# Optimization experiments

Hardware: AMD Instinct MI355X
Metric: run time of the kernel (lower is better)

Reference implementation:

```python
import jax, jax.numpy as jnp
import numpy as np

K_LEN, I_LEN, DIM = 1024, 8192, 128


def setup_inputs() -> dict:
    key = jax.random.key(0)
    k1, k2 = jax.random.split(key)
    kernel = jax.random.normal(k1, (K_LEN, DIM), dtype=jnp.float32)
    x = jax.random.normal(k2, (I_LEN, DIM), dtype=jnp.float32)
    return {"kernel": kernel, "x": x}


def _cost_matrix(kernel, x):
    # squared Euclidean pairwise distances, (K, I), via GEMM form
    k2 = jnp.sum(kernel * kernel, axis=-1)  # (K,)
    x2 = jnp.sum(x * x, axis=-1)            # (I,)
    c = k2[:, None] + x2[None, :] - 2.0 * (kernel @ x.T)
    return jnp.maximum(c, 0.0)


def _acc_matrix(c):
    # DTW DP: D[i,j] = c[i,j] + min(D[i-1,j-1], D[i-1,j], D[i,j-1])
    # Row recurrence solved per-row with a (min,+) prefix scan:
    #   e[j] = min(D_prev[j-1], D_prev[j]) + c[j]   (e[0] = D_prev[0] + c[0])
    #   D[j] = S[j] + cummin(e - S),  S = cumsum(c_row)
    row0 = jnp.cumsum(c[0])

    def step(prev, c_row):
        m = jnp.concatenate([prev[:1], jnp.minimum(prev[:-1], prev[1:])])
        e = m + c_row
        S = jnp.cumsum(c_row)
        row = S + jax.lax.cummin(e - S)
        return row, row

    _, rows = jax.lax.scan(step, row0, c[1:])
    return jnp.concatenate([row0[None, :], rows], axis=0)  # (K, I)


def _backtrack(D):
    # tslearn-style backtracking from (K-1, I-1) to (0, 0).
    # Candidate order [diag, up, left]; argmin ties pick first (diag),
    # matching numpy.argmin used by tslearn. Out-of-range -> +inf border.
    K, I = D.shape
    Dp = jnp.full((K + 1, I + 1), jnp.inf, dtype=D.dtype).at[1:, 1:].set(D)
    L = K + I - 1  # max possible path length

    def step(carry, _):
        k, i, fin = carry
        emit = (k, i, jnp.logical_not(fin))
        fin2 = fin | ((k == 0) & (i == 0))
        cand = jnp.stack([Dp[k, i], Dp[k, i + 1], Dp[k + 1, i]])
        a = jnp.argmin(cand)
        nk = jnp.where(fin2, k, k - (a != 2).astype(k.dtype))
        ni = jnp.where(fin2, i, i - (a != 1).astype(i.dtype))
        return (nk, ni, fin2), emit

    init = (jnp.int32(K - 1), jnp.int32(I - 1), jnp.bool_(False))
    _, (ks, iss, valid) = jax.lax.scan(step, init, None, length=L)
    return ks, iss, valid


def reference(kernel, x):
    # Path search uses detached tensors in the original module.
    c = jax.lax.stop_gradient(_cost_matrix(kernel, x))
    D = _acc_matrix(c)
    ks, iss, valid = _backtrack(D)
    # sum of squared diffs along the optimal alignment path (gather + reduce)
    d2 = jnp.sum((kernel[ks] - x[iss]) ** 2, axis=-1)  # (L,)
    return jnp.sum(jnp.where(valid, d2, 0.0))
```

## Files before the change

kernel.cpp:

```cpp
#include <hip/hip_runtime.h>
#include <hip/hip_bf16.h>

typedef unsigned short ushort_t;
typedef unsigned int uint_t;

#define KL 1024
#define IL 8192
#define DIMV 128
#define NS 16
#define NB 258
#define NIT 269
#define SSH (8256*64)
#define GATE 416
#define INF __builtin_inff()

typedef __attribute__((ext_vector_type(8))) short v8s;
typedef __attribute__((ext_vector_type(4))) float v4f;

__global__ __launch_bounds__(256) void knorms(
    const float* __restrict__ kern, const float* __restrict__ xx,
    float* __restrict__ x2, float* __restrict__ k2, int* __restrict__ flags) {
  if (blockIdx.x == 0 && threadIdx.x < NS) flags[threadIdx.x] = 0;
  const int lane = threadIdx.x & 63;
  const int row = blockIdx.x * 4 + (threadIdx.x >> 6);
  const float* src;
  float* dst;
  if (row < IL) { src = xx + (size_t)row * DIMV; dst = x2 + row; }
  else          { src = kern + (size_t)(row - IL) * DIMV; dst = k2 + (row - IL); }
  float2 v = *(const float2*)(src + lane * 2);
  float ss = v.x * v.x + v.y * v.y;
  #pragma unroll
  for (int off = 32; off > 0; off >>= 1) ss += __shfl_down(ss, off, 64);
  if (lane == 0) *dst = ss;
}

__device__ __forceinline__ v8s pack_bf16x8(float4 a, float4 b) {
  union { unsigned int u[4]; v8s v; } r;
  union { __hip_bfloat162 h; unsigned int u; } t;
  t.h = __float22bfloat162_rn(make_float2(a.x, a.y)); r.u[0] = t.u;
  t.h = __float22bfloat162_rn(make_float2(a.z, a.w)); r.u[1] = t.u;
  t.h = __float22bfloat162_rn(make_float2(b.x, b.y)); r.u[2] = t.u;
  t.h = __float22bfloat162_rn(make_float2(b.z, b.w)); r.u[3] = t.u;
  return r.v;
}

__global__ __launch_bounds__(256) void kgemm(
    const float* __restrict__ kern, const float* __restrict__ xx,
    const float* __restrict__ x2, const float* __restrict__ k2,
    ushort_t* __restrict__ c_h) {
  __shared__ float ctile[64 * 64];
  const int T = threadIdx.x;
  const int w = T >> 6;
  const int lane = T & 63;
  const int lo = lane & 15;
  const int hi = lane >> 4;
  const int i0 = blockIdx.x * 64;
  const int s  = blockIdx.y;
  const int kr0 = s * 64;

  v4f acc[4] = {};
  #pragma unroll
  for (int ks = 0; ks < 4; ks++) {
    const int k = ks * 32 + hi * 8;
    const float* bp = xx + (size_t)(i0 + w * 16 + lo) * DIMV + k;
    v8s bf = pack_bf16x8(*(const float4*)bp, *(const float4*)(bp + 4));
    #pragma unroll
    for (int rt = 0; rt < 4; rt++) {
      const float* ap = kern + (size_t)(kr0 + rt * 16 + lo) * DIMV + k;
      v8s af = pack_bf16x8(*(const float4*)ap, *(const float4*)(ap + 4));
      acc[rt] = __builtin_amdgcn_mfma_f32_16x16x32_bf16(af, bf, acc[rt], 0, 0, 0);
    }
  }
  const float x2v = x2[i0 + w * 16 + lo];
  const int n_local = w * 16 + lo;
  #pragma unroll
  for (int rt = 0; rt < 4; rt++) {
    float4 k2f = *(const float4*)&k2[kr0 + rt * 16 + hi * 4];
    #pragma unroll
    for (int q = 0; q < 4; q++) {
      const int m_local = rt * 16 + hi * 4 + q;
      float cval = fmaxf((&k2f.x)[q] + x2v - 2.f * acc[rt][q], 0.f);
      ctile[n_local * 64 + ((m_local + 2 * n_local) & 63)] = cval;
    }
  }
  __syncthreads();
  _Float16* ob = (_Float16*)(c_h + (size_t)s * SSH);
  #pragma unroll
  for (int q = 0; q < 32; q++) {
    int tt = w + q * 4;
    int di = tt - lane;
    if (tt <= 126 && di >= 0 && di < 64) {
      int t = i0 + tt;
      ob[((size_t)(t >> 1) * 64 + lane) * 2 + (t & 1)] =
          (_Float16)ctile[di * 64 + ((lane + 2 * di) & 63)];
    }
  }
}

__device__ __forceinline__ float dpp_wave_shr1(float oldv, float src) {
  return __int_as_float(__builtin_amdgcn_update_dpp(
      __float_as_int(oldv), __float_as_int(src), 0x138, 0xF, 0xF, false));
}
__device__ __forceinline__ float dpp_wave_rol1(float src) {
  return __int_as_float(__builtin_amdgcn_update_dpp(
      __float_as_int(src), __float_as_int(src), 0x134, 0xF, 0xF, false));
}
__device__ __forceinline__ float dpp_wave_shl1(float oldv, float src) {
  return __int_as_float(__builtin_amdgcn_update_dpp(
      __float_as_int(oldv), __float_as_int(src), 0x130, 0xF, 0xF, false));
}

__global__ __launch_bounds__(384) void kdp(
    const ushort_t* __restrict__ c_h, float* __restrict__ bound,
    int* __restrict__ flags, float* __restrict__ out) {
  __shared__ uint_t cbuf[4 * 2 * 1024];
  __shared__ float ring[4 * 4 * 32];
  __shared__ float feed[4 * 32];
  const int g = blockIdx.x;
  const int wv = threadIdx.x >> 6;
  const int lane = threadIdx.x & 63;
  const int sb = g * 4;

  float Dcur = INF, Dul = INF, Bout = INF;
  int fchk = 0, fpend = 0;
  float rfeed = INF;
  const float* bin = bound + (size_t)(sb > 0 ? sb - 1 : 0) * IL;
  float* bout3 = bound + (size_t)(sb + 3) * IL;

  if (wv == 4) {
    const char* gs = (const char*)(c_h + (size_t)sb * SSH);
    uint_t* dst = cbuf;
    #pragma unroll
    for (int q = 0; q < 4; q++)
      __builtin_amdgcn_global_load_lds(
          (const __attribute__((address_space(1))) void*)(gs + (size_t)q * 1024 + lane * 16),
          (__attribute__((address_space(3))) void*)(dst + q * 256 + lane * 4), 16, 0, 0);
  } else if (wv == 5) {
    if (g > 0) {
      int f;
      do { f = __hip_atomic_load(&flags[sb - 1], __ATOMIC_RELAXED, __HIP_MEMORY_SCOPE_AGENT); } while (f < GATE);
      fchk = f; fpend = f;
      if (lane < 32) {
        feed[lane]      = __hip_atomic_load(&bin[lane],      __ATOMIC_RELAXED, __HIP_MEMORY_SCOPE_AGENT);
        feed[32 + lane] = __hip_atomic_load(&bin[32 + lane], __ATOMIC_RELAXED, __HIP_MEMORY_SCOPE_AGENT);
        rfeed           = __hip_atomic_load(&bin[64 + lane], __ATOMIC_RELAXED, __HIP_MEMORY_SCOPE_AGENT);
      }
    } else {
      if (lane < 32) { feed[lane] = INF; feed[32+lane] = INF; feed[64+lane] = INF; feed[96+lane] = INF; }
    }
  } else if (wv < 4) {
    if (g == 0 && wv == 0 && lane == 0) Dcur = 0.f;
  }
  __syncthreads();

  for (int i = 0; i < NIT; i++) {
    if (wv < 4) {
      const int W = i - 3 * wv;
      if (W >= 0 && W < NB) {
        const uint_t* lc = cbuf + (wv * 2 + (W & 1)) * 1024 + lane;
        uint_t lv[16];
        #pragma unroll
        for (int tp = 0; tp < 16; tp++) lv[tp] = lc[tp * 64];
        float Bv = (wv == 0) ? feed[(W & 3) * 32 + (lane & 31)]
                             : ring[(wv - 1) * 128 + (W & 3) * 32 + (lane & 31)];
        float cvv[32];
        #pragma unroll
        for (int tp = 0; tp < 16; tp++) {
          union { uint_t u; _Float16 h[2]; } cu; cu.u = lv[tp];
          cvv[2 * tp]     = (float)cu.h[0];
          cvv[2 * tp + 1] = (float)cu.h[1];
        }
        if (W >= 2 && W < 256) {
          #pragma unroll
          for (int tt = 0; tt < 32; tt++) {
            float Dup = dpp_wave_shr1(Bv, Dcur);
            float m1 = fminf(Dul, Dcur);
            Bv = dpp_wave_rol1(Bv);
            Dcur = cvv[tt] + fminf(m1, Dup);
            Dul = Dup;
            Bout = dpp_wave_shl1(Dcur, Bout);
          }
        } else {
          const int t0 = W * 32;
          #pragma unroll
          for (int tt = 0; tt < 32; tt++) {
            const int t = t0 + tt;
            float Dup = dpp_wave_shr1(Bv, Dcur);
            float m1 = fminf(Dul, Dcur);
            Bv = dpp_wave_rol1(Bv);
            float Dnew = cvv[tt] + fminf(m1, Dup);
            const bool alo = (t >= lane);
            const bool ahi = (t - lane < IL);
            if (alo) Dul = Dup;
            if (alo && ahi) Dcur = Dnew;
            Bout = dpp_wave_shl1(Dcur, Bout);
          }
        }
        if (lane >= 32) {
          const int slot = (lane == 63) ? (W - 1) : (W - 2);
          if (slot >= 0)
            ring[wv * 128 + ((slot & 3) << 5) + ((lane + 1) & 31)] = Bout;
        }
      }
    } else if (wv == 4) {
      #pragma unroll
      for (int k = 0; k < 4; k++) {
        const int B = i + 1 - 3 * k;
        if (B >= 0 && B < NB) {
          const char* gs = (const char*)(c_h + (size_t)(sb + k) * SSH) + (size_t)B * 4096;
          uint_t* dst = cbuf + (k * 2 + (B & 1)) * 1024;
          #pragma unroll
          for (int q = 0; q < 4; q++)
            __builtin_amdgcn_global_load_lds(
                (const __attribute__((address_space(1))) void*)(gs + (size_t)q * 1024 + lane * 16),
                (__attribute__((address_space(3))) void*)(dst + q * 256 + lane * 4), 16, 0, 0);
        }
      }
    } else {
      if (g > 0) {
        if (fpend > fchk) fchk = fpend;
        const int Fw = i + 2;
        if (Fw >= 2 && Fw <= 255 && lane < 32) feed[(Fw & 3) * 32 + lane] = rfeed;
        const int Fl = i + 3;
        if (Fl <= 255) {
          const int need = 32 * (Fl + 1);
          if (fchk < need) {
            int f;
            do { f = __hip_atomic_load(&flags[sb - 1], __ATOMIC_RELAXED, __HIP_MEMORY_SCOPE_AGENT); } while (f < need);
            fchk = f;
          }
          if (lane < 32)
            rfeed = __hip_atomic_load(&bin[32 * Fl + lane], __ATOMIC_RELAXED, __HIP_MEMORY_SCOPE_AGENT);
        }
        fpend = __hip_atomic_load(&flags[sb - 1], __ATOMIC_RELAXED, __HIP_MEMORY_SCOPE_AGENT);
      }
      if (g < 3) {
        const int E = i - 12;
        if (E >= 0 && E < 256 && lane < 32) {
          float bv2 = ring[3 * 128 + (E & 3) * 32 + lane];
          __hip_atomic_store(&bout3[32 * E + lane], bv2, __ATOMIC_RELAXED, __HIP_MEMORY_SCOPE_AGENT);
        }
        const int Ep = i - 13;
        if (Ep >= 0 && Ep < 256 && lane == 0)
          __hip_atomic_store(&flags[sb + 3], 32 * Ep + 32, __ATOMIC_RELAXED, __HIP_MEMORY_SCOPE_AGENT);
      }
    }
    __syncthreads();
  }
  if (g == 3 && wv == 3 && lane == 63) out[0] = Dcur;
}

extern "C" void kernel_launch(void* const* d_in, const int* in_sizes, int n_in,
                              void* d_out, int out_size, void* d_ws, size_t ws_size,
                              hipStream_t stream) {
  const float* kern = (const float*)d_in[0];
  const float* xx   = (const float*)d_in[1];
  char* ws = (char*)d_ws;
  const size_t OFF_X2 = (size_t)NS * SSH * 2;
  const size_t OFF_K2 = OFF_X2 + (size_t)IL * 4;
  const size_t OFF_BD = OFF_K2 + (size_t)KL * 4;
  const size_t OFF_FL = OFF_BD + (size_t)NS * IL * 4;
  ushort_t* c_h  = (ushort_t*)ws;
  float* x2    = (float*)(ws + OFF_X2);
  float* k2    = (float*)(ws + OFF_K2);
  float* bnd   = (float*)(ws + OFF_BD);
  int*   flags = (int*)(ws + OFF_FL);

  knorms<<<(IL + KL) / 4, 256, 0, stream>>>(kern, xx, x2, k2, flags);
  kgemm<<<dim3(IL / 64, NS), 256, 0, stream>>>(kern, xx, x2, k2, c_h);
  kdp<<<4, 384, 0, stream>>>(c_h, bnd, flags, (float*)d_out);
}
```

Measured before the change: 405.3 us.

## Replace per-iteration block barriers with LDS flag-based producer/consumer sync in DP kernel

The DP wavefront kernel no longer advances every wave in lockstep with __syncthreads each iteration. Each compute, loader, feed and export wave now runs its own loop and waits on per-stage counters in LDS. The cost buffer goes from double to triple buffering, and a seventh wave splits off boundary export from boundary feeding. This removes barrier stalls where one slow wave holds up all others. In exchange it adds spin-polling on LDS and needs careful memory ordering, which risks races or hangs if any flag dependency is wrong.

```diff
diff --git a/kernel.cpp b/kernel.cpp
--- a/kernel.cpp
+++ b/kernel.cpp
@@ -9,10 +9,16 @@
 #define DIMV 128
 #define NS 16
 #define NB 258
-#define NIT 269
+#define NR 267
 #define SSH (8256*64)
 #define GATE 416
+#define BIGF 0x3fffffff
 #define INF __builtin_inff()
+
+#define CF 0
+#define PF 4
+#define GF 8
+#define EF 9
 
 typedef __attribute__((ext_vector_type(8))) short v8s;
 typedef __attribute__((ext_vector_type(4))) float v4f;
@@ -110,144 +116,166 @@
       __float_as_int(oldv), __float_as_int(src), 0x130, 0xF, 0xF, false));
 }
 
-__global__ __launch_bounds__(384) void kdp(
+__device__ __forceinline__ int lds_poll_ge(int* p, int need, int cached) {
+  if (cached >= need) return cached;
+  int f;
+  do { f = __hip_atomic_load(p, __ATOMIC_RELAXED, __HIP_MEMORY_SCOPE_WORKGROUP); } while (f < need);
+  return f;
+}
+
+__global__ __launch_bounds__(448) void kdp(
     const ushort_t* __restrict__ c_h, float* __restrict__ bound,
     int* __restrict__ flags, float* __restrict__ out) {
-  __shared__ uint_t cbuf[4 * 2 * 1024];
+  __shared__ uint_t cbuf[13 * 1024];
   __shared__ float ring[4 * 4 * 32];
-  __shared__ float feed[4 * 32];
+  __shared__ float feedb[4 * 32];
+  __shared__ int flg[16];
   const int g = blockIdx.x;
   const int wv = threadIdx.x >> 6;
   const int lane = threadIdx.x & 63;
   const int sb = g * 4;
 
-  float Dcur = INF, Dul = INF, Bout = INF;
-  int fchk = 0, fpend = 0;
-  float rfeed = INF;
-  const float* bin = bound + (size_t)(sb > 0 ? sb - 1 : 0) * IL;
-  float* bout3 = bound + (size_t)(sb + 3) * IL;
-
-  if (wv == 4) {
-    const char* gs = (const char*)(c_h + (size_t)sb * SSH);
-    uint_t* dst = cbuf;
+  if (threadIdx.x < 16) {
+    int v = -1;
+    if (threadIdx.x == GF && g == 0) v = BIGF;
+    if (threadIdx.x == EF && g == 3) v = BIGF;
+    flg[threadIdx.x] = v;
+  }
+  if (wv == 1) { feedb[lane] = INF; feedb[64 + lane] = INF; }
+  __syncthreads();
+
+  if (wv < 4) {
+    const int k = wv;
+    float Dcur = (g == 0 && k == 0 && lane == 0) ? 0.f : INF;
+    float Dul = INF, Bout = INF;
+    int fc = -1, fp = -1;
+    int fe = (g == 3 && k == 3) ? BIGF : -1;
+    int s3 = 0;
+    for (int W = 0; W < NB; W++) {
+      fc = lds_poll_ge(&flg[CF + k], W, fc);
+      if (k == 0) {
+        if (W < 256) fp = lds_poll_ge(&flg[GF], W, fp);
+      } else {
+        int pn = W + 2; if (pn > 257) pn = 257;
+        fp = lds_poll_ge(&flg[PF + k - 1], pn, fp);
+      }
+      fe = lds_poll_ge(&flg[(k < 3) ? (PF + k + 1) : EF], W - 4, fe);
+      const uint_t* lc = cbuf + (k * 3 + s3) * 1024 + lane;
+      uint_t lv[16];
+      #pragma unroll
+      for (int tp = 0; tp < 16; tp++) lv[tp] = lc[tp * 64];
+      float Bv = (k == 0) ? feedb[(W & 3) * 32 + (lane & 31)]
+                          : ring[(k - 1) * 128 + (W & 3) * 32 + (lane & 31)];
+      float cvv[32];
+      #pragma unroll
+      for (int tp = 0; tp < 16; tp++) {
+        union { uint_t u; _Float16 h[2]; } cu; cu.u = lv[tp];
+        cvv[2 * tp]     = (float)cu.h[0];
+        cvv[2 * tp + 1] = (float)cu.h[1];
+      }
+      if (W >= 2 && W < 256) {
+        #pragma unroll
+        for (int tt = 0; tt < 32; tt++) {
+          float Dup = dpp_wave_shr1(Bv, Dcur);
+          float m1 = fminf(Dul, Dcur);
+          Bv = dpp_wave_rol1(Bv);
+          Dcur = cvv[tt] + fminf(m1, Dup);
+          Dul = Dup;
+          Bout = dpp_wave_shl1(Dcur, Bout);
+        }
+      } else {
+        const int t0 = W * 32;
+        #pragma unroll
+        for (int tt = 0; tt < 32; tt++) {
+          const int t = t0 + tt;
+          float Dup = dpp_wave_shr1(Bv, Dcur);
+          float m1 = fminf(Dul, Dcur);
+          Bv = dpp_wave_rol1(Bv);
+          float Dnew = cvv[tt] + fminf(m1, Dup);
+          const bool alo = (t >= lane);
+          const bool ahi = (t - lane < IL);
+          if (alo) Dul = Dup;
+          if (alo && ahi) Dcur = Dnew;
+          Bout = dpp_wave_shl1(Dcur, Bout);
+        }
+      }
+      if (lane >= 32) {
+        const int slot = (lane == 63) ? (W - 1) : (W - 2);
+        if (slot >= 0) ring[k * 128 + ((slot & 3) << 5) + ((lane + 1) & 31)] = Bout;
+      }
+      __hip_atomic_store(&flg[PF + k], W, __ATOMIC_RELEASE, __HIP_MEMORY_SCOPE_WORKGROUP);
+      s3 = (s3 == 2) ? 0 : s3 + 1;
+    }
+    if (g == 3 && k == 3 && lane == 63) out[0] = Dcur;
+  } else if (wv == 4) {
+    int fpk[4] = {-1, -1, -1, -1};
+    for (int R = 0; R < NR; R++) {
+      const int sl = R % 3;
+      #pragma unroll
+      for (int k = 0; k < 4; k++) {
+        const int B = R - 3 * k;
+        const bool v = (B >= 0) && (B < NB);
+        if (v) fpk[k] = lds_poll_ge(&flg[PF + k], B - 3, fpk[k]);
+        const int slot = v ? (k * 3 + sl) : 12;
+        const char* src = (const char*)(c_h + (size_t)(sb + k) * SSH) + (size_t)(v ? B : 0) * 4096;
+        uint_t* dst = cbuf + slot * 1024;
+        #pragma unroll
+        for (int q = 0; q < 4; q++)
+          __builtin_amdgcn_global_load_lds(
+              (const __attribute__((address_space(1))) void*)(src + (size_t)q * 1024 + lane * 16),
+              (__attribute__((address_space(3))) void*)(dst + q * 256 + lane * 4), 16, 0, 0);
+      }
+      asm volatile("s_waitcnt vmcnt(16)" ::: "memory");
+      #pragma unroll
+      for (int k = 0; k < 4; k++) {
+        int c = (R - 1) - 3 * k; if (c > 257) c = 257;
+        if (c >= 0)
+          __hip_atomic_store(&flg[CF + k], c, __ATOMIC_RELAXED, __HIP_MEMORY_SCOPE_WORKGROUP);
+      }
+    }
+    asm volatile("s_waitcnt vmcnt(0)" ::: "memory");
     #pragma unroll
-    for (int q = 0; q < 4; q++)
-      __builtin_amdgcn_global_load_lds(
-          (const __attribute__((address_space(1))) void*)(gs + (size_t)q * 1024 + lane * 16),
-          (__attribute__((address_space(3))) void*)(dst + q * 256 + lane * 4), 16, 0, 0);
+    for (int k = 0; k < 4; k++)
+      __hip_atomic_store(&flg[CF + k], 257, __ATOMIC_RELAXED, __HIP_MEMORY_SCOPE_WORKGROUP);
   } else if (wv == 5) {
     if (g > 0) {
-      int f;
-      do { f = __hip_atomic_load(&flags[sb - 1], __ATOMIC_RELAXED, __HIP_MEMORY_SCOPE_AGENT); } while (f < GATE);
-      fchk = f; fpend = f;
-      if (lane < 32) {
-        feed[lane]      = __hip_atomic_load(&bin[lane],      __ATOMIC_RELAXED, __HIP_MEMORY_SCOPE_AGENT);
-        feed[32 + lane] = __hip_atomic_load(&bin[32 + lane], __ATOMIC_RELAXED, __HIP_MEMORY_SCOPE_AGENT);
-        rfeed           = __hip_atomic_load(&bin[64 + lane], __ATOMIC_RELAXED, __HIP_MEMORY_SCOPE_AGENT);
-      }
-    } else {
-      if (lane < 32) { feed[lane] = INF; feed[32+lane] = INF; feed[64+lane] = INF; feed[96+lane] = INF; }
-    }
-  } else if (wv < 4) {
-    if (g == 0 && wv == 0 && lane == 0) Dcur = 0.f;
-  }
-  __syncthreads();
-
-  for (int i = 0; i < NIT; i++) {
-    if (wv < 4) {
-      const int W = i - 3 * wv;
-      if (W >= 0 && W < NB) {
-        const uint_t* lc = cbuf + (wv * 2 + (W & 1)) * 1024 + lane;
-        uint_t lv[16];
-        #pragma unroll
-        for (int tp = 0; tp < 16; tp++) lv[tp] = lc[tp * 64];
-        float Bv = (wv == 0) ? feed[(W & 3) * 32 + (lane & 31)]
-                             : ring[(wv - 1) * 128 + (W & 3) * 32 + (lane & 31)];
-        float cvv[32];
-        #pragma unroll
-        for (int tp = 0; tp < 16; tp++) {
-          union { uint_t u; _Float16 h[2]; } cu; cu.u = lv[tp];
-          cvv[2 * tp]     = (float)cu.h[0];
-          cvv[2 * tp + 1] = (float)cu.h[1];
+      const float* bin = bound + (size_t)(sb - 1) * IL;
+      int fg;
+      do { fg = __hip_atomic_load(&flags[sb - 1], __ATOMIC_RELAXED, __HIP_MEMORY_SCOPE_AGENT); } while (fg < GATE);
+      int fp0 = -1;
+      for (int F = 0; F <= 254; F += 2) {
+        const int need = 32 * F + 64;
+        while (fg < need)
+          fg = __hip_atomic_load(&flags[sb - 1], __ATOMIC_RELAXED, __HIP_MEMORY_SCOPE_AGENT);
+        float r = __hip_atomic_load(&bin[32 * F + lane], __ATOMIC_RELAXED, __HIP_MEMORY_SCOPE_AGENT);
+        fp0 = lds_poll_ge(&flg[PF + 0], F - 3, fp0);
+        feedb[(F & 3) * 32 + lane] = r;
+        __hip_atomic_store(&flg[GF], F + 1, __ATOMIC_RELEASE, __HIP_MEMORY_SCOPE_WORKGROUP);
+      }
+    }
+  } else {
+    if (g < 3) {
+      float* bout3 = bound + (size_t)(sb + 3) * IL;
+      int fp3 = -1;
+      for (int E = 0; E < 256; E++) {
+        int pn = E + 2; if (pn > 257) pn = 257;
+        fp3 = lds_poll_ge(&flg[PF + 3], pn, fp3);
+        float bv = ring[3 * 128 + (E & 3) * 32 + (lane & 31)];
+        asm volatile("s_waitcnt lgkmcnt(0)" ::: "memory");
+        __hip_atomic_store(&flg[EF], E, __ATOMIC_RELAXED, __HIP_MEMORY_SCOPE_WORKGROUP);
+        if (lane < 32)
+          __hip_atomic_store(&bout3[32 * E + lane], bv, __ATOMIC_RELAXED, __HIP_MEMORY_SCOPE_AGENT);
+        if (E >= 2) {
+          asm volatile("s_waitcnt vmcnt(3)" ::: "memory");
+          if (lane == 0)
+            __hip_atomic_store(&flags[sb + 3], 32 * (E - 2) + 32, __ATOMIC_RELAXED, __HIP_MEMORY_SCOPE_AGENT);
         }
-        if (W >= 2 && W < 256) {
-          #pragma unroll
-          for (int tt = 0; tt < 32; tt++) {
-            float Dup = dpp_wave_shr1(Bv, Dcur);
-            float m1 = fminf(Dul, Dcur);
-            Bv = dpp_wave_rol1(Bv);
-            Dcur = cvv[tt] + fminf(m1, Dup);
-            Dul = Dup;
-            Bout = dpp_wave_shl1(Dcur, Bout);
-          }
-        } else {
-          const int t0 = W * 32;
-          #pragma unroll
-          for (int tt = 0; tt < 32; tt++) {
-            const int t = t0 + tt;
-            float Dup = dpp_wave_shr1(Bv, Dcur);
-            float m1 = fminf(Dul, Dcur);
-            Bv = dpp_wave_rol1(Bv);
-            float Dnew = cvv[tt] + fminf(m1, Dup);
-            const bool alo = (t >= lane);
-            const bool ahi = (t - lane < IL);
-            if (alo) Dul = Dup;
-            if (alo && ahi) Dcur = Dnew;
-            Bout = dpp_wave_shl1(Dcur, Bout);
-          }
-        }
-        if (lane >= 32) {
-          const int slot = (lane == 63) ? (W - 1) : (W - 2);
-          if (slot >= 0)
-            ring[wv * 128 + ((slot & 3) << 5) + ((lane + 1) & 31)] = Bout;
-        }
-      }
-    } else if (wv == 4) {
-      #pragma unroll
-      for (int k = 0; k < 4; k++) {
-        const int B = i + 1 - 3 * k;
-        if (B >= 0 && B < NB) {
-          const char* gs = (const char*)(c_h + (size_t)(sb + k) * SSH) + (size_t)B * 4096;
-          uint_t* dst = cbuf + (k * 2 + (B & 1)) * 1024;
-          #pragma unroll
-          for (int q = 0; q < 4; q++)
-            __builtin_amdgcn_global_load_lds(
-                (const __attribute__((address_space(1))) void*)(gs + (size_t)q * 1024 + lane * 16),
-                (__attribute__((address_space(3))) void*)(dst + q * 256 + lane * 4), 16, 0, 0);
-        }
-      }
-    } else {
-      if (g > 0) {
-        if (fpend > fchk) fchk = fpend;
-        const int Fw = i + 2;
-        if (Fw >= 2 && Fw <= 255 && lane < 32) feed[(Fw & 3) * 32 + lane] = rfeed;
-        const int Fl = i + 3;
-        if (Fl <= 255) {
-          const int need = 32 * (Fl + 1);
-          if (fchk < need) {
-            int f;
-            do { f = __hip_atomic_load(&flags[sb - 1], __ATOMIC_RELAXED, __HIP_MEMORY_SCOPE_AGENT); } while (f < need);
-            fchk = f;
-          }
-          if (lane < 32)
-            rfeed = __hip_atomic_load(&bin[32 * Fl + lane], __ATOMIC_RELAXED, __HIP_MEMORY_SCOPE_AGENT);
-        }
-        fpend = __hip_atomic_load(&flags[sb - 1], __ATOMIC_RELAXED, __HIP_MEMORY_SCOPE_AGENT);
-      }
-      if (g < 3) {
-        const int E = i - 12;
-        if (E >= 0 && E < 256 && lane < 32) {
-          float bv2 = ring[3 * 128 + (E & 3) * 32 + lane];
-          __hip_atomic_store(&bout3[32 * E + lane], bv2, __ATOMIC_RELAXED, __HIP_MEMORY_SCOPE_AGENT);
-        }
-        const int Ep = i - 13;
-        if (Ep >= 0 && Ep < 256 && lane == 0)
-          __hip_atomic_store(&flags[sb + 3], 32 * Ep + 32, __ATOMIC_RELAXED, __HIP_MEMORY_SCOPE_AGENT);
-      }
-    }
-    __syncthreads();
-  }
-  if (g == 3 && wv == 3 && lane == 63) out[0] = Dcur;
+      }
+      asm volatile("s_waitcnt vmcnt(0)" ::: "memory");
+      if (lane == 0)
+        __hip_atomic_store(&flags[sb + 3], IL, __ATOMIC_RELAXED, __HIP_MEMORY_SCOPE_AGENT);
+    }
+  }
 }
 
 extern "C" void kernel_launch(void* const* d_in, const int* in_sizes, int n_in,
@@ -268,5 +296,5 @@
 
   knorms<<<(IL + KL) / 4, 256, 0, stream>>>(kern, xx, x2, k2, flags);
   kgemm<<<dim3(IL / 64, NS), 256, 0, stream>>>(kern, xx, x2, k2, c_h);
-  kdp<<<4, 384, 0, stream>>>(c_h, bnd, flags, (float*)d_out);
-}
+  kdp<<<4, 448, 0, stream>>>(c_h, bnd, flags, (float*)d_out);
+}
```

Result: slower. 595.7 us (+47.0%).
